# Kernel optimization log

Hardware: AMD Instinct MI355X
Metric: run time of the kernel (lower is better)

## Reference

```python
import jax, jax.numpy as jnp
import numpy as np

N_CLASS, EMB, HID = 32000, 256, 512
B, T = 256, 256


def setup_inputs() -> dict:
    key = jax.random.key(0)
    ks = iter(jax.random.split(key, 64))

    def g(shape, scale=0.02):
        return jax.random.normal(next(ks), shape, jnp.float32) * scale

    inp = {
        "X": jax.random.randint(next(ks), (B, T), 0, N_CLASS),
        "H": g((B, HID)),
        "C": g((B, HID)),
        "E": g((N_CLASS, EMB)),
    }
    # two stacked LSTM cells, gates i/f/o/c; weights stored [in, out] so y = x @ W
    for name in ["i", "f", "o", "c"]:
        inp["W_x" + name] = g((EMB, HID))
        inp["W_h" + name] = g((HID, HID))
        inp["b_" + name] = jnp.ones((HID,), jnp.float32)
        inp["W_x" + name + "1"] = g((EMB, HID))
        inp["W_h" + name + "1"] = g((HID, HID))
        inp["b_" + name + "1"] = jnp.ones((HID,), jnp.float32)
    inp["W_xh"] = g((HID, HID))
    inp["W_hh"] = g((HID, HID))
    inp["b_h"] = jnp.ones((HID,), jnp.float32)
    inp["W_hq"] = g((HID, N_CLASS))
    inp["b_q"] = jnp.ones((N_CLASS,), jnp.float32)
    return inp


def reference(X, H, C, E,
              W_xi, W_hi, b_i, W_xf, W_hf, b_f, W_xo, W_ho, b_o, W_xc, W_hc, b_c,
              W_xi1, W_hi1, b_i1, W_xf1, W_hf1, b_f1, W_xo1, W_ho1, b_o1, W_xc1, W_hc1, b_c1,
              W_xh, W_hh, b_h, W_hq, b_q):
    xs = jnp.swapaxes(E[X], 0, 1)  # [T, B, EMB] time-major, like X.transpose(0,1)

    def step(carry, x_t):
        H, C, H1, C1 = carry
        # first LSTM cell
        I = jax.nn.sigmoid(x_t @ W_xi + H @ W_hi + b_i)
        F = jax.nn.sigmoid(x_t @ W_xf + H @ W_hf + b_f)
        O = jax.nn.sigmoid(x_t @ W_xo + H @ W_ho + b_o)
        Ct = jnp.tanh(x_t @ W_xc + H @ W_hc + b_c)
        C = F * C + I * Ct
        H = O * jnp.tanh(C)
        # inter-layer gated mix (note: H1 is overwritten before the 2nd cell, as in the original)
        H1 = jax.nn.sigmoid(H @ W_xh + H1 @ W_hh + b_h)
        # second LSTM cell
        I1 = jax.nn.sigmoid(x_t @ W_xi1 + H1 @ W_hi1 + b_i1)
        F1 = jax.nn.sigmoid(x_t @ W_xf1 + H1 @ W_hf1 + b_f1)
        O1 = jax.nn.sigmoid(x_t @ W_xo1 + H1 @ W_ho1 + b_o1)
        Ct1 = jnp.tanh(x_t @ W_xc1 + H1 @ W_hc1 + b_c1)
        C1 = F1 * C1 + I1 * Ct1
        H1 = O1 * jnp.tanh(C1)
        return (H, C, H1, C1), None

    # H1 and C1 are initialized from H and C (H1 = H; C1 = C in the original)
    (H, C, H1, C1), _ = jax.lax.scan(step, (H, C, H, C), xs)
    return H1 @ W_hq + b_q  # [B, N_CLASS]
```

## Files before the change

### kernel.cpp

```cpp
#include <hip/hip_runtime.h>
#include <cstdint>
#include <cstddef>

typedef unsigned short u16;
typedef unsigned long long u64;
typedef __attribute__((ext_vector_type(8))) short s16x8;
typedef __attribute__((ext_vector_type(4))) float f32x4;
typedef __attribute__((ext_vector_type(4))) unsigned short u16x4;

#define AGENT __HIP_MEMORY_SCOPE_AGENT

namespace {
constexpr int NWG  = 256;
constexpr int NTHR = 256;
constexpr int Bb   = 256;
constexpr int Tt   = 256;
constexpr int EMB_ = 256;
constexpr int HID_ = 512;
constexpr int NCLS = 32000;

constexpr int OFF_W1  = 0;
constexpr int OFF_W3  = 49152;
constexpr int OFF_W2  = 98304;
constexpr int OFF_DS  = 131072;
constexpr int OFF_DS1 = 139520;
constexpr int OFF_DSM = 147968;
constexpr int OFF_C   = 150144;
constexpr int OFF_C1  = 152192;
constexpr int OFF_B1  = 154240;
constexpr int OFF_B3  = 154368;
constexpr int OFF_B2  = 154496;
constexpr int SMEM_BYTES = 154560;

constexpr size_t WS_FL   = 0;
constexpr size_t WS_DONE = 32768;
constexpr size_t WS_HB0  = 33792;
constexpr size_t WS_HB1  = WS_HB0 + (size_t)Bb * HID_ * 2;
constexpr size_t WS_H1   = WS_HB1 + (size_t)Bb * HID_ * 2;
constexpr size_t WS_HM   = WS_H1 + (size_t)Bb * HID_ * 2;
constexpr size_t WS_XE   = WS_HM + (size_t)Bb * HID_ * 2;
}

struct Params {
  const int* X; const float* Hin; const float* Cin; const float* E;
  const float* Wx[4];  const float* Wh[4];  const float* bg[4];
  const float* Wx1[4]; const float* Wh1[4]; const float* bg1[4];
  const float* Wxh; const float* Whh; const float* bh;
  const float* Whq; const float* bq;
  float* out; char* ws;
};

__device__ __forceinline__ u16 f2bf(float f) {
  union { float f; unsigned u; } v; v.f = f;
  unsigned r = v.u + 0x7FFFu + ((v.u >> 16) & 1u);
  return (u16)(r >> 16);
}
__device__ __forceinline__ float sigm(float x) { return 1.f / (1.f + __expf(-x)); }
__device__ __forceinline__ float tanh_(float x) {
  x = fminf(fmaxf(x, -10.f), 10.f);
  float e = __expf(-2.f * x);
  return (1.f - e) / (1.f + e);
}
__device__ __forceinline__ f32x4 mfma16(s16x8 a, s16x8 b, f32x4 c) {
  return __builtin_amdgcn_mfma_f32_16x16x32_bf16(a, b, c, 0, 0, 0);
}

__device__ __forceinline__ void st8_llc(u16* p2, u64 v) {
  __hip_atomic_store((u64*)p2, v, __ATOMIC_RELAXED, AGENT);
}

#define LD16A(d, b, off)                                                      \
  asm volatile("global_load_dwordx4 %0, %1, off offset:" #off " sc0 sc1"      \
               : "=&v"(d) : "v"(b) : "memory")

__device__ __forceinline__ void ld_h16(s16x8* d, const u16* b) {
  LD16A(d[0],  b, 0);   LD16A(d[1],  b, 64);  LD16A(d[2],  b, 128);
  LD16A(d[3],  b, 192); LD16A(d[4],  b, 256); LD16A(d[5],  b, 320);
  LD16A(d[6],  b, 384); LD16A(d[7],  b, 448); LD16A(d[8],  b, 512);
  LD16A(d[9],  b, 576); LD16A(d[10], b, 640); LD16A(d[11], b, 704);
  LD16A(d[12], b, 768); LD16A(d[13], b, 832); LD16A(d[14], b, 896);
  LD16A(d[15], b, 960);
}
__device__ __forceinline__ void ld_h8a(s16x8* d, const u16* b) {
  LD16A(d[0], b, 0);   LD16A(d[1], b, 64);  LD16A(d[2], b, 128);
  LD16A(d[3], b, 192); LD16A(d[4], b, 256); LD16A(d[5], b, 320);
  LD16A(d[6], b, 384); LD16A(d[7], b, 448);
}
__device__ __forceinline__ void ld_h8b(s16x8* d, const u16* b) {
  LD16A(d[8],  b, 512); LD16A(d[9],  b, 576); LD16A(d[10], b, 640);
  LD16A(d[11], b, 704); LD16A(d[12], b, 768); LD16A(d[13], b, 832);
  LD16A(d[14], b, 896); LD16A(d[15], b, 960);
}
__device__ __forceinline__ void waitld() {
  asm volatile("s_waitcnt vmcnt(0)" ::: "memory");
  __builtin_amdgcn_sched_barrier(0);
}
#define WAITLDN(n) do {                                                       \
  asm volatile("s_waitcnt vmcnt(" #n ")" ::: "memory");                       \
  __builtin_amdgcn_sched_barrier(0); } while (0)

__device__ __forceinline__ void arrive_cnt(int* fl, int c) {
  __syncthreads();
  if (threadIdx.x == 0)
    (void)__hip_atomic_fetch_add(&fl[(c & 7) * 32 + 16], 1, __ATOMIC_RELAXED, AGENT);
}
__device__ __forceinline__ void wait_cnt(int* fl, int ph) {
  const int tgt = ph * 8;
  if (threadIdx.x < 8) {
    for (;;) {
      int v = __hip_atomic_load(&fl[threadIdx.x * 32 + 16], __ATOMIC_RELAXED, AGENT);
      if (!__any(v < tgt)) break;
      __builtin_amdgcn_s_sleep(1);
    }
  }
  __syncthreads();
  __builtin_amdgcn_fence(__ATOMIC_ACQUIRE, "workgroup");
}

__device__ __forceinline__ void groupbar_heavy(int* fl, int slot, int ph) {
  __syncthreads();
  if (threadIdx.x == 0)
    __hip_atomic_store(&fl[slot * 32], ph, __ATOMIC_RELEASE, AGENT);
  if (threadIdx.x < 64) {
    for (;;) {
      int v = __hip_atomic_load(&fl[threadIdx.x * 32], __ATOMIC_RELAXED, AGENT);
      if (!__any(v < ph)) break;
      __builtin_amdgcn_s_sleep(1);
    }
  }
  __syncthreads();
  __builtin_amdgcn_fence(__ATOMIC_ACQUIRE, "agent");
}

__device__ __forceinline__ void donebar(int* dn, int bi) {
  __syncthreads();
  if (threadIdx.x == 0)
    __hip_atomic_store(&dn[bi], 1, __ATOMIC_RELEASE, AGENT);
  for (;;) {
    int v = __hip_atomic_load(&dn[threadIdx.x], __ATOMIC_RELAXED, AGENT);
    if (!__any(v < 1)) break;
    __builtin_amdgcn_s_sleep(1);
  }
  __syncthreads();
  __builtin_amdgcn_fence(__ATOMIC_ACQUIRE, "agent");
}

__device__ __forceinline__ void cell_phase(char* smem, int offW, int offB, int offC,
                                           const u16* Xt, const u16* Hrec, u16* Hdst,
                                           int g, int c, int w, int lane, int tid) {
  const int r = lane & 15, q = lane >> 4;
  const int row0 = w * 16;
  const u16* xrow = Xt + (size_t)(g * 64 + row0 + r) * EMB_;
  const u16* hrow = Hrec + (size_t)(g * 64 + row0 + r) * HID_;
  const u16* wb = (const u16*)(smem + offW) + lane * 8;
  f32x4 acc0 = {0.f, 0.f, 0.f, 0.f}, acc1 = {0.f, 0.f, 0.f, 0.f};
#pragma unroll
  for (int kb = 0; kb < 8; kb++) {
    s16x8 a  = *(const s16x8*)(xrow + kb * 32 + q * 8);
    s16x8 b0 = *(const s16x8*)(wb + (size_t)(kb * 2 + 0) * 512);
    s16x8 b1 = *(const s16x8*)(wb + (size_t)(kb * 2 + 1) * 512);
    acc0 = mfma16(a, b0, acc0);
    acc1 = mfma16(a, b1, acc1);
  }
  s16x8 ha[16];
  ld_h16(ha, hrow + q * 8);
  waitld();
#pragma unroll
  for (int kb = 0; kb < 16; kb++) {
    s16x8 b0 = *(const s16x8*)(wb + (size_t)((kb + 8) * 2 + 0) * 512);
    s16x8 b1 = *(const s16x8*)(wb + (size_t)((kb + 8) * 2 + 1) * 512);
    acc0 = mfma16(ha[kb], b0, acc0);
    acc1 = mfma16(ha[kb], b1, acc1);
  }
  float* Ds = (float*)(smem + OFF_DS);
#pragma unroll
  for (int i = 0; i < 4; i++) {
    Ds[(row0 + q * 4 + i) * 33 + r]      = acc0[i];
    Ds[(row0 + q * 4 + i) * 33 + 16 + r] = acc1[i];
  }
  __syncthreads();
  const float* bs = (const float*)(smem + offB);
  float* Cs = (float*)(smem + offC);
  if (tid < 128) {
    int row = tid >> 1, j0 = (tid & 1) * 4;
    union { u16 h[4]; u64 qv; } pk;
#pragma unroll
    for (int i = 0; i < 4; i++) {
      int j = j0 + i;
      float vi = Ds[row * 33 + 0 + j]  + bs[0 + j];
      float vf = Ds[row * 33 + 8 + j]  + bs[8 + j];
      float vo = Ds[row * 33 + 16 + j] + bs[16 + j];
      float vc = Ds[row * 33 + 24 + j] + bs[24 + j];
      float I = sigm(vi), F = sigm(vf), O = sigm(vo), Ct = tanh_(vc);
      float Cn = F * Cs[row * 8 + j] + I * Ct;
      Cs[row * 8 + j] = Cn;
      pk.h[i] = f2bf(O * tanh_(Cn));
    }
    st8_llc(Hdst + (size_t)(g * 64 + row) * HID_ + c * 8 + j0, pk.qv);
  }
}

__device__ __forceinline__ void cell1_w23(char* smem, const u16* Xt, const u16* Hrec,
                                          u16* Hdst, int g, int c, int lane, int tid) {
  const int wv = (tid >> 6) - 2;
  const int r = lane & 15, q = lane >> 4;
  const u16* wb1 = (const u16*)(smem + OFF_W1) + lane * 8;
  float* D1 = (float*)(smem + OFF_DS1);
#pragma unroll
  for (int blk = 0; blk < 2; blk++) {
    const int rb = wv * 32 + blk * 16;
    const u16* xrow = Xt + (size_t)(g * 64 + rb + r) * EMB_;
    const u16* hrow = Hrec + (size_t)(g * 64 + rb + r) * HID_;
    s16x8 xa[8];
#pragma unroll
    for (int kb = 0; kb < 8; kb++) xa[kb] = *(const s16x8*)(xrow + kb * 32 + q * 8);
    s16x8 hh[16];
    ld_h8a(hh, hrow + q * 8);
    f32x4 a0 = {0.f, 0.f, 0.f, 0.f}, a1 = {0.f, 0.f, 0.f, 0.f};
#pragma unroll
    for (int kb = 0; kb < 8; kb++) {
      a0 = mfma16(xa[kb], *(const s16x8*)(wb1 + (size_t)(kb * 2 + 0) * 512), a0);
      a1 = mfma16(xa[kb], *(const s16x8*)(wb1 + (size_t)(kb * 2 + 1) * 512), a1);
    }
    waitld();
#pragma unroll
    for (int kb = 0; kb < 8; kb++) {
      a0 = mfma16(hh[kb], *(const s16x8*)(wb1 + (size_t)((kb + 8) * 2 + 0) * 512), a0);
      a1 = mfma16(hh[kb], *(const s16x8*)(wb1 + (size_t)((kb + 8) * 2 + 1) * 512), a1);
    }
    ld_h8b(hh, hrow + q * 8);
    waitld();
#pragma unroll
    for (int kb = 8; kb < 16; kb++) {
      a0 = mfma16(hh[kb], *(const s16x8*)(wb1 + (size_t)((kb + 8) * 2 + 0) * 512), a0);
      a1 = mfma16(hh[kb], *(const s16x8*)(wb1 + (size_t)((kb + 8) * 2 + 1) * 512), a1);
    }
#pragma unroll
    for (int i = 0; i < 4; i++) {
      D1[(rb + q * 4 + i) * 33 + r]      = a0[i];
      D1[(rb + q * 4 + i) * 33 + 16 + r] = a1[i];
    }
  }
  const float* bs = (const float*)(smem + OFF_B1);
  float* Cs = (float*)(smem + OFF_C);
  int t2 = tid - 128;
  int row = t2 >> 1, j0 = (t2 & 1) * 4;
  union { u16 h[4]; u64 qv; } pk;
#pragma unroll
  for (int i = 0; i < 4; i++) {
    int j = j0 + i;
    float vi = D1[row * 33 + 0 + j]  + bs[0 + j];
    float vf = D1[row * 33 + 8 + j]  + bs[8 + j];
    float vo = D1[row * 33 + 16 + j] + bs[16 + j];
    float vc = D1[row * 33 + 24 + j] + bs[24 + j];
    float I = sigm(vi), F = sigm(vf), O = sigm(vo), Ct = tanh_(vc);
    float Cn = F * Cs[row * 8 + j] + I * Ct;
    Cs[row * 8 + j] = Cn;
    pk.h[i] = f2bf(O * tanh_(Cn));
  }
  st8_llc(Hdst + (size_t)(g * 64 + row) * HID_ + c * 8 + j0, pk.qv);
}

__device__ __forceinline__ f32x4 mix_part1(char* smem, const u16* Hnew, int g, int c,
                                           int w, int lane) {
  const int r = lane & 15, q = lane >> 4;
  int rbase = g * 64 + (c & 1) * 32 + w * 16 + r;
  const u16* h0 = Hnew + (size_t)rbase * HID_;
  const u16* wb = (const u16*)(smem + OFF_W2) + lane * 8;
  s16x8 ha[16];
  f32x4 acc = {0.f, 0.f, 0.f, 0.f};
  ld_h8a(ha, h0 + q * 8);
  waitld();
#pragma unroll
  for (int kb = 0; kb < 8; kb++)
    acc = mfma16(ha[kb], *(const s16x8*)(wb + (size_t)kb * 512), acc);
  ld_h8b(ha, h0 + q * 8);
  waitld();
#pragma unroll
  for (int kb = 8; kb < 16; kb++)
    acc = mfma16(ha[kb], *(const s16x8*)(wb + (size_t)kb * 512), acc);
  return acc;
}

__device__ __forceinline__ void mix_part2(char* smem, f32x4 acc, const u16* H1old,
                                          u16* H1m, int g, int c, int w, int lane) {
  const int r = lane & 15, q = lane >> 4;
  int rbase = g * 64 + (c & 1) * 32 + w * 16 + r;
  const u16* h1 = H1old + (size_t)rbase * HID_;
  const u16* wb = (const u16*)(smem + OFF_W2) + lane * 8;
  s16x8 hb[16];
  ld_h16(hb, h1 + q * 8);
  __builtin_amdgcn_sched_barrier(0);
  WAITLDN(12);
#pragma unroll
  for (int kb = 0; kb < 4; kb++)
    acc = mfma16(hb[kb], *(const s16x8*)(wb + (size_t)(16 + kb) * 512), acc);
  WAITLDN(8);
#pragma unroll
  for (int kb = 4; kb < 8; kb++)
    acc = mfma16(hb[kb], *(const s16x8*)(wb + (size_t)(16 + kb) * 512), acc);
  WAITLDN(4);
#pragma unroll
  for (int kb = 8; kb < 12; kb++)
    acc = mfma16(hb[kb], *(const s16x8*)(wb + (size_t)(16 + kb) * 512), acc);
  WAITLDN(0);
#pragma unroll
  for (int kb = 12; kb < 16; kb++)
    acc = mfma16(hb[kb], *(const s16x8*)(wb + (size_t)(16 + kb) * 512), acc);
  float* Dm = (float*)(smem + OFF_DSM) + (size_t)w * 16 * 17;
#pragma unroll
  for (int i = 0; i < 4; i++) Dm[(q * 4 + i) * 17 + r] = acc[i];
  const float* b2 = (const float*)(smem + OFF_B2);
  int row2 = lane >> 2, j0 = (lane & 3) * 4;
  union { u16 h[4]; u64 qv; } pk;
#pragma unroll
  for (int i = 0; i < 4; i++)
    pk.h[i] = f2bf(sigm(Dm[row2 * 17 + j0 + i] + b2[j0 + i]));
  st8_llc(H1m + (size_t)(g * 64 + (c & 1) * 32 + w * 16 + row2) * HID_ + (c >> 1) * 16 + j0,
          pk.qv);
}

__global__ __launch_bounds__(NTHR, 1) void lstm_pers(Params p) {
  extern __shared__ char smem[];
  const int tid = threadIdx.x;
  const int bi = blockIdx.x;
  const int w = tid >> 6, lane = tid & 63;
  const int g = bi >> 6, c = bi & 63;
  const int r = lane & 15, q = lane >> 4;

  int* fl = (int*)(p.ws + WS_FL) + g * 64 * 32;
  int* dn = (int*)(p.ws + WS_DONE);
  u16* Hb0 = (u16*)(p.ws + WS_HB0);
  u16* Hb1 = (u16*)(p.ws + WS_HB1);
  u16* H1b = (u16*)(p.ws + WS_H1);
  u16* H1m = (u16*)(p.ws + WS_HM);
  u16* Xe  = (u16*)(p.ws + WS_XE);

  if (tid == 0 && c < 8)
    __hip_atomic_store(&fl[c * 32 + 16], 0, __ATOMIC_RELAXED, AGENT);

  {
    u16* w1 = (u16*)(smem + OFF_W1);
    u16* w3 = (u16*)(smem + OFF_W3);
    int gate = tid >> 6, kk8 = (tid >> 3) & 7, j = tid & 7;
    int cc = gate * 8 + j;
    int n = cc >> 4, rr = cc & 15;
    int hid = c * 8 + j;
    for (int kk = kk8; kk < 768; kk += 8) {
      int kb = kk >> 5, q2 = (kk >> 3) & 3, e = kk & 7;
      size_t dst = ((size_t)(kb * 2 + n) * 64 + q2 * 16 + rr) * 8 + e;
      float s1 = (kk < 256) ? p.Wx[gate][(size_t)kk * HID_ + hid]
                            : p.Wh[gate][(size_t)(kk - 256) * HID_ + hid];
      float s3 = (kk < 256) ? p.Wx1[gate][(size_t)kk * HID_ + hid]
                            : p.Wh1[gate][(size_t)(kk - 256) * HID_ + hid];
      w1[dst] = f2bf(s1);
      w3[dst] = f2bf(s3);
    }
    {
      u16* w2 = (u16*)(smem + OFF_W2);
      int kk16 = tid >> 4, j2 = tid & 15;
      int hid2 = (c >> 1) * 16 + j2;
      for (int kk = kk16; kk < 1024; kk += 16) {
        int kb = kk >> 5, q2 = (kk >> 3) & 3, e = kk & 7;
        size_t dst = ((size_t)kb * 64 + q2 * 16 + j2) * 8 + e;
        float s = (kk < 512) ? p.Wxh[(size_t)kk * HID_ + hid2]
                             : p.Whh[(size_t)(kk - 512) * HID_ + hid2];
        w2[dst] = f2bf(s);
      }
      if (tid < 16) ((float*)(smem + OFF_B2))[tid] = p.bh[(c >> 1) * 16 + tid];
    }
    if (tid < 32) {
      int gt = tid >> 3, jj = tid & 7;
      ((float*)(smem + OFF_B1))[tid] = p.bg[gt][c * 8 + jj];
      ((float*)(smem + OFF_B3))[tid] = p.bg1[gt][c * 8 + jj];
    }
    float* Cs = (float*)(smem + OFF_C);
    float* C1s = (float*)(smem + OFF_C1);
    for (int it = 0; it < 2; it++) {
      int idx = tid + it * 256;
      int row = idx >> 3, j8 = idx & 7;
      float v = p.Cin[(size_t)(g * 64 + row) * HID_ + c * 8 + j8];
      Cs[row * 8 + j8] = v;
      C1s[row * 8 + j8] = v;
    }
  }
  for (int it = 0; it < 2; it++) {
    int idx = bi * 512 + tid + it * 256;
    u16 hv = f2bf(p.Hin[idx]);
    Hb1[idx] = hv;
    H1b[idx] = hv;
  }
  for (int tt = 0; tt < 4; tt++) {
    int t0 = c * 4 + tt;
    for (int pp = 0; pp < 16; pp++) {
      int b = g * 64 + w * 16 + pp;
      int tok = p.X[(size_t)b * Tt + t0];
      const float4* er = (const float4*)(p.E + (size_t)tok * EMB_);
      float4 v = er[lane];
      u16x4 u; u.x = f2bf(v.x); u.y = f2bf(v.y); u.z = f2bf(v.z); u.w = f2bf(v.w);
      *(u16x4*)(Xe + ((size_t)t0 * Bb + b) * EMB_ + lane * 4) = u;
    }
  }
  groupbar_heavy(fl, c, 1);

  int cph = 0;

  cell_phase(smem, OFF_W1, OFF_B1, OFF_C, Xe, Hb1, Hb0, g, c, w, lane, tid);
  arrive_cnt(fl, c); ++cph;

  wait_cnt(fl, cph);
  if (w < 2) {
    f32x4 macc = mix_part1(smem, Hb0, g, c, w, lane);
    mix_part2(smem, macc, H1b, H1m, g, c, w, lane);
  } else {
    cell1_w23(smem, Xe + (size_t)1 * Bb * EMB_, Hb0, Hb1, g, c, lane, tid);
  }
  arrive_cnt(fl, c); ++cph;

  for (int t = 0; t < Tt - 1; t++) {
    const u16* Xt = Xe + (size_t)t * Bb * EMB_;
    {
      const u16* wb3 = (const u16*)(smem + OFF_W3) + lane * 8;
      const u16* xrow = Xt + (size_t)(g * 64 + w * 16 + r) * EMB_;
      f32x4 acc0 = {0.f, 0.f, 0.f, 0.f}, acc1 = {0.f, 0.f, 0.f, 0.f};
      s16x8 xa[8];
#pragma unroll
      for (int kb = 0; kb < 8; kb++) xa[kb] = *(const s16x8*)(xrow + kb * 32 + q * 8);
#pragma unroll
      for (int kb = 0; kb < 8; kb++) {
        acc0 = mfma16(xa[kb], *(const s16x8*)(wb3 + (size_t)(kb * 2 + 0) * 512), acc0);
        acc1 = mfma16(xa[kb], *(const s16x8*)(wb3 + (size_t)(kb * 2 + 1) * 512), acc1);
      }
      wait_cnt(fl, cph);
      const u16* hrow = H1m + (size_t)(g * 64 + w * 16 + r) * HID_;
      s16x8 ha[16];
      ld_h16(ha, hrow + q * 8);
      __builtin_amdgcn_sched_barrier(0);
      WAITLDN(12);
#pragma unroll
      for (int kb = 0; kb < 4; kb++) {
        acc0 = mfma16(ha[kb], *(const s16x8*)(wb3 + (size_t)((kb + 8) * 2 + 0) * 512), acc0);
        acc1 = mfma16(ha[kb], *(const s16x8*)(wb3 + (size_t)((kb + 8) * 2 + 1) * 512), acc1);
      }
      WAITLDN(8);
#pragma unroll
      for (int kb = 4; kb < 8; kb++) {
        acc0 = mfma16(ha[kb], *(const s16x8*)(wb3 + (size_t)((kb + 8) * 2 + 0) * 512), acc0);
        acc1 = mfma16(ha[kb], *(const s16x8*)(wb3 + (size_t)((kb + 8) * 2 + 1) * 512), acc1);
      }
      WAITLDN(4);
#pragma unroll
      for (int kb = 8; kb < 12; kb++) {
        acc0 = mfma16(ha[kb], *(const s16x8*)(wb3 + (size_t)((kb + 8) * 2 + 0) * 512), acc0);
        acc1 = mfma16(ha[kb], *(const s16x8*)(wb3 + (size_t)((kb + 8) * 2 + 1) * 512), acc1);
      }
      WAITLDN(0);
#pragma unroll
      for (int kb = 12; kb < 16; kb++) {
        acc0 = mfma16(ha[kb], *(const s16x8*)(wb3 + (size_t)((kb + 8) * 2 + 0) * 512), acc0);
        acc1 = mfma16(ha[kb], *(const s16x8*)(wb3 + (size_t)((kb + 8) * 2 + 1) * 512), acc1);
      }
      float* Ds = (float*)(smem + OFF_DS);
#pragma unroll
      for (int i = 0; i < 4; i++) {
        Ds[(w * 16 + q * 4 + i) * 33 + r]      = acc0[i];
        Ds[(w * 16 + q * 4 + i) * 33 + 16 + r] = acc1[i];
      }
      __syncthreads();
      if (tid < 128) {
        const float* bs = (const float*)(smem + OFF_B3);
        float* Cs = (float*)(smem + OFF_C1);
        int row = tid >> 1, j0 = (tid & 1) * 4;
        union { u16 h[4]; u64 qv; } pk;
#pragma unroll
        for (int i = 0; i < 4; i++) {
          int j = j0 + i;
          float vi = Ds[row * 33 + 0 + j]  + bs[0 + j];
          float vf = Ds[row * 33 + 8 + j]  + bs[8 + j];
          float vo = Ds[row * 33 + 16 + j] + bs[16 + j];
          float vc = Ds[row * 33 + 24 + j] + bs[24 + j];
          float I = sigm(vi), F = sigm(vf), O = sigm(vo), Ct = tanh_(vc);
          float Cn = F * Cs[row * 8 + j] + I * Ct;
          Cs[row * 8 + j] = Cn;
          pk.h[i] = f2bf(O * tanh_(Cn));
        }
        st8_llc(H1b + (size_t)(g * 64 + row) * HID_ + c * 8 + j0, pk.qv);
      }
      arrive_cnt(fl, c); ++cph;
    }
    {
      const u16* Hnew = (t & 1) ? Hb0 : Hb1;
      u16* Hdst1      = (t & 1) ? Hb1 : Hb0;
      f32x4 macc = {0.f, 0.f, 0.f, 0.f};
      if (w < 2) {
        macc = mix_part1(smem, Hnew, g, c, w, lane);
      } else if (t + 2 < Tt) {
        cell1_w23(smem, Xe + (size_t)(t + 2) * Bb * EMB_, Hnew, Hdst1, g, c, lane, tid);
      }
      wait_cnt(fl, cph);
      if (w < 2) mix_part2(smem, macc, H1b, H1m, g, c, w, lane);
      arrive_cnt(fl, c); ++cph;
    }
  }

  {
    const u16* Xt = Xe + (size_t)(Tt - 1) * Bb * EMB_;
    const u16* wb3 = (const u16*)(smem + OFF_W3) + lane * 8;
    const u16* xrow = Xt + (size_t)(g * 64 + w * 16 + r) * EMB_;
    f32x4 acc0 = {0.f, 0.f, 0.f, 0.f}, acc1 = {0.f, 0.f, 0.f, 0.f};
    s16x8 xa[8];
#pragma unroll
    for (int kb = 0; kb < 8; kb++) xa[kb] = *(const s16x8*)(xrow + kb * 32 + q * 8);
#pragma unroll
    for (int kb = 0; kb < 8; kb++) {
      acc0 = mfma16(xa[kb], *(const s16x8*)(wb3 + (size_t)(kb * 2 + 0) * 512), acc0);
      acc1 = mfma16(xa[kb], *(const s16x8*)(wb3 + (size_t)(kb * 2 + 1) * 512), acc1);
    }
    wait_cnt(fl, cph);
    const u16* hrow = H1m + (size_t)(g * 64 + w * 16 + r) * HID_;
    s16x8 ha[16];
    ld_h16(ha, hrow + q * 8);
    waitld();
#pragma unroll
    for (int kb = 0; kb < 16; kb++) {
      acc0 = mfma16(ha[kb], *(const s16x8*)(wb3 + (size_t)((kb + 8) * 2 + 0) * 512), acc0);
      acc1 = mfma16(ha[kb], *(const s16x8*)(wb3 + (size_t)((kb + 8) * 2 + 1) * 512), acc1);
    }
    float* Ds = (float*)(smem + OFF_DS);
#pragma unroll
    for (int i = 0; i < 4; i++) {
      Ds[(w * 16 + q * 4 + i) * 33 + r]      = acc0[i];
      Ds[(w * 16 + q * 4 + i) * 33 + 16 + r] = acc1[i];
    }
    __syncthreads();
    if (tid < 128) {
      const float* bs = (const float*)(smem + OFF_B3);
      float* Cs = (float*)(smem + OFF_C1);
      int row = tid >> 1, j0 = (tid & 1) * 4;
      union { u16 h[4]; u64 qv; } pk;
#pragma unroll
      for (int i = 0; i < 4; i++) {
        int j = j0 + i;
        float vi = Ds[row * 33 + 0 + j]  + bs[0 + j];
        float vf = Ds[row * 33 + 8 + j]  + bs[8 + j];
        float vo = Ds[row * 33 + 16 + j] + bs[16 + j];
        float vc = Ds[row * 33 + 24 + j] + bs[24 + j];
        float I = sigm(vi), F = sigm(vf), O = sigm(vo), Ct = tanh_(vc);
        float Cn = F * Cs[row * 8 + j] + I * Ct;
        Cs[row * 8 + j] = Cn;
        pk.h[i] = f2bf(O * tanh_(Cn));
      }
      st8_llc(H1b + (size_t)(g * 64 + row) * HID_ + c * 8 + j0, pk.qv);
    }
  }

  donebar(dn, bi);
  if (bi < 250) {
    const int n0 = bi * 128;
    u16* Wf = (u16*)smem;
    for (int idx = tid; idx < 512 * 128; idx += NTHR) {
      int k = idx >> 7, nn2 = idx & 127;
      int nt = nn2 >> 4, rr = nn2 & 15;
      int kb = k >> 5, q2 = (k >> 3) & 3, e = k & 7;
      Wf[((size_t)(kb * 8 + nt) * 64 + q2 * 16 + rr) * 8 + e] =
          f2bf(p.Whq[(size_t)k * NCLS + n0 + nn2]);
    }
    float* bqs = (float*)(smem + OFF_C);
    if (tid < 128) bqs[tid] = p.bq[n0 + tid];
    __syncthreads();
    const int r2 = lane & 15, q2 = lane >> 4;
    for (int mt = 0; mt < 4; mt++) {
      int rowb = mt * 64 + w * 16;
      const u16* arow = H1b + (size_t)(rowb + r2) * HID_;
      f32x4 acc[8];
#pragma unroll
      for (int nt = 0; nt < 8; nt++) acc[nt] = (f32x4){0.f, 0.f, 0.f, 0.f};
      for (int kb = 0; kb < 16; kb++) {
        s16x8 a = *(const s16x8*)(arow + kb * 32 + q2 * 8);
#pragma unroll
        for (int nt = 0; nt < 8; nt++) {
          s16x8 b = *(const s16x8*)((const u16*)Wf + ((size_t)(kb * 8 + nt) * 64 + lane) * 8);
          acc[nt] = mfma16(a, b, acc[nt]);
        }
      }
#pragma unroll
      for (int nt = 0; nt < 8; nt++)
#pragma unroll
        for (int i = 0; i < 4; i++)
          p.out[(size_t)(rowb + q2 * 4 + i) * NCLS + n0 + nt * 16 + r2] =
              acc[nt][i] + bqs[nt * 16 + r2];
    }
  }
}

extern "C" void kernel_launch(void* const* d_in, const int* in_sizes, int n_in,
                              void* d_out, int out_size, void* d_ws, size_t ws_size,
                              hipStream_t stream) {
  (void)in_sizes; (void)n_in; (void)out_size; (void)ws_size;
  Params p;
  p.X   = (const int*)d_in[0];
  p.Hin = (const float*)d_in[1];
  p.Cin = (const float*)d_in[2];
  p.E   = (const float*)d_in[3];
  for (int gidx = 0; gidx < 4; gidx++) {
    int base = 4 + gidx * 6;
    p.Wx[gidx]  = (const float*)d_in[base + 0];
    p.Wh[gidx]  = (const float*)d_in[base + 1];
    p.bg[gidx]  = (const float*)d_in[base + 2];
    p.Wx1[gidx] = (const float*)d_in[base + 3];
    p.Wh1[gidx] = (const float*)d_in[base + 4];
    p.bg1[gidx] = (const float*)d_in[base + 5];
  }
  p.Wxh = (const float*)d_in[28];
  p.Whh = (const float*)d_in[29];
  p.bh  = (const float*)d_in[30];
  p.Whq = (const float*)d_in[31];
  p.bq  = (const float*)d_in[32];
  p.out = (float*)d_out;
  p.ws  = (char*)d_ws;

  hipFuncSetAttribute(reinterpret_cast<const void*>(lstm_pers),
                      hipFuncAttributeMaxDynamicSharedMemorySize, SMEM_BYTES);
  lstm_pers<<<dim3(NWG), dim3(NTHR), SMEM_BYTES, stream>>>(p);
}
```

Before: 3.399 ms.

## Quantize inter-layer hidden states H1 and mix output to uint8 with fp16 MFMA

The second-layer hidden state and the gated mix output are stored as 8-bit unsigned codes (affine for H1, scaled for the sigmoid mix) instead of bf16. Consumers decode the bytes to fp16 and run fp16 MFMAs against fp16 weights, then apply the scale. The zero-point offset is folded into the biases via precomputed column sums of the weights. This halves the bytes exchanged between workgroups on every recurrent step, which targets the latency-bound cross-workgroup traffic, at the cost of extra decode instructions and considerably lower numerical precision.

```diff
diff --git a/kernel.cpp b/kernel.cpp
--- a/kernel.cpp
+++ b/kernel.cpp
@@ -3,9 +3,12 @@
 #include <cstddef>
 
 typedef unsigned short u16;
+typedef unsigned char u8;
 typedef unsigned long long u64;
 typedef __attribute__((ext_vector_type(8))) short s16x8;
+typedef __attribute__((ext_vector_type(8))) _Float16 f16x8;
 typedef __attribute__((ext_vector_type(4))) float f32x4;
+typedef __attribute__((ext_vector_type(4))) unsigned int u32x4;
 typedef __attribute__((ext_vector_type(4))) unsigned short u16x4;
 
 #define AGENT __HIP_MEMORY_SCOPE_AGENT
@@ -18,6 +21,9 @@
 constexpr int EMB_ = 256;
 constexpr int HID_ = 512;
 constexpr int NCLS = 32000;
+
+constexpr float S_HM = 1.0f / 255.0f;
+constexpr float S_H1 = 1.0f / 127.5f;
 
 constexpr int OFF_W1  = 0;
 constexpr int OFF_W3  = 49152;
@@ -36,9 +42,9 @@
 constexpr size_t WS_DONE = 32768;
 constexpr size_t WS_HB0  = 33792;
 constexpr size_t WS_HB1  = WS_HB0 + (size_t)Bb * HID_ * 2;
-constexpr size_t WS_H1   = WS_HB1 + (size_t)Bb * HID_ * 2;
-constexpr size_t WS_HM   = WS_H1 + (size_t)Bb * HID_ * 2;
-constexpr size_t WS_XE   = WS_HM + (size_t)Bb * HID_ * 2;
+constexpr size_t WS_H18  = WS_HB1 + (size_t)Bb * HID_ * 2;
+constexpr size_t WS_HM8  = WS_H18 + (size_t)Bb * HID_;
+constexpr size_t WS_XE   = WS_HM8 + (size_t)Bb * HID_;
 }
 
 struct Params {
@@ -55,6 +61,10 @@
   unsigned r = v.u + 0x7FFFu + ((v.u >> 16) & 1u);
   return (u16)(r >> 16);
 }
+__device__ __forceinline__ u16 f2h(float f) {
+  _Float16 h = (_Float16)f;
+  union { _Float16 h; u16 u; } v; v.h = h; return v.u;
+}
 __device__ __forceinline__ float sigm(float x) { return 1.f / (1.f + __expf(-x)); }
 __device__ __forceinline__ float tanh_(float x) {
   x = fminf(fmaxf(x, -10.f), 10.f);
@@ -64,11 +74,42 @@
 __device__ __forceinline__ f32x4 mfma16(s16x8 a, s16x8 b, f32x4 c) {
   return __builtin_amdgcn_mfma_f32_16x16x32_bf16(a, b, c, 0, 0, 0);
 }
+__device__ __forceinline__ f32x4 mfma16h(f16x8 a, f16x8 b, f32x4 c) {
+  return __builtin_amdgcn_mfma_f32_16x16x32_f16(a, b, c, 0, 0, 0);
+}
+
+__device__ __forceinline__ int permk(int k) {
+  return ((k >> 6) << 6) | (((k >> 3) & 3) << 4) | (((k >> 5) & 1) << 3) | (k & 7);
+}
+
+__device__ __forceinline__ f16x8 dec8(unsigned lo, unsigned hi) {
+  union { unsigned w[4]; f16x8 v; } o;
+  float a, b;
+  asm("v_cvt_f32_ubyte0 %0, %1" : "=v"(a) : "v"(lo));
+  asm("v_cvt_f32_ubyte1 %0, %1" : "=v"(b) : "v"(lo));
+  asm("v_cvt_pkrtz_f16_f32 %0, %1, %2" : "=v"(o.w[0]) : "v"(a), "v"(b));
+  asm("v_cvt_f32_ubyte2 %0, %1" : "=v"(a) : "v"(lo));
+  asm("v_cvt_f32_ubyte3 %0, %1" : "=v"(b) : "v"(lo));
+  asm("v_cvt_pkrtz_f16_f32 %0, %1, %2" : "=v"(o.w[1]) : "v"(a), "v"(b));
+  asm("v_cvt_f32_ubyte0 %0, %1" : "=v"(a) : "v"(hi));
+  asm("v_cvt_f32_ubyte1 %0, %1" : "=v"(b) : "v"(hi));
+  asm("v_cvt_pkrtz_f16_f32 %0, %1, %2" : "=v"(o.w[2]) : "v"(a), "v"(b));
+  asm("v_cvt_f32_ubyte2 %0, %1" : "=v"(a) : "v"(hi));
+  asm("v_cvt_f32_ubyte3 %0, %1" : "=v"(b) : "v"(hi));
+  asm("v_cvt_pkrtz_f16_f32 %0, %1, %2" : "=v"(o.w[3]) : "v"(a), "v"(b));
+  return o.v;
+}
+__device__ __forceinline__ unsigned enc4(float a, float b, float c2, float d) {
+  unsigned ua = (unsigned)a, ub = (unsigned)b, uc = (unsigned)c2, ud = (unsigned)d;
+  return ua | (ub << 8) | (uc << 16) | (ud << 24);
+}
 
 __device__ __forceinline__ void st8_llc(u16* p2, u64 v) {
   __hip_atomic_store((u64*)p2, v, __ATOMIC_RELAXED, AGENT);
 }
-
+__device__ __forceinline__ void st4_llc(u8* pb, unsigned v) {
+  __hip_atomic_store((unsigned*)pb, v, __ATOMIC_RELAXED, AGENT);
+}
 #define LD16A(d, b, off)                                                      \
   asm volatile("global_load_dwordx4 %0, %1, off offset:" #off " sc0 sc1"      \
                : "=&v"(d) : "v"(b) : "memory")
@@ -91,6 +132,11 @@
   LD16A(d[11], b, 704); LD16A(d[12], b, 768); LD16A(d[13], b, 832);
   LD16A(d[14], b, 896); LD16A(d[15], b, 960);
 }
+__device__ __forceinline__ void ld_u8x8(u32x4* d, const u8* b) {
+  LD16A(d[0], b, 0);   LD16A(d[1], b, 64);  LD16A(d[2], b, 128);
+  LD16A(d[3], b, 192); LD16A(d[4], b, 256); LD16A(d[5], b, 320);
+  LD16A(d[6], b, 384); LD16A(d[7], b, 448);
+}
 __device__ __forceinline__ void waitld() {
   asm volatile("s_waitcnt vmcnt(0)" ::: "memory");
   __builtin_amdgcn_sched_barrier(0);
@@ -116,7 +162,6 @@
   __syncthreads();
   __builtin_amdgcn_fence(__ATOMIC_ACQUIRE, "workgroup");
 }
-
 __device__ __forceinline__ void groupbar_heavy(int* fl, int slot, int ph) {
   __syncthreads();
   if (threadIdx.x == 0)
@@ -131,7 +176,6 @@
   __syncthreads();
   __builtin_amdgcn_fence(__ATOMIC_ACQUIRE, "agent");
 }
-
 __device__ __forceinline__ void donebar(int* dn, int bi) {
   __syncthreads();
   if (threadIdx.x == 0)
@@ -157,20 +201,16 @@
 #pragma unroll
   for (int kb = 0; kb < 8; kb++) {
     s16x8 a  = *(const s16x8*)(xrow + kb * 32 + q * 8);
-    s16x8 b0 = *(const s16x8*)(wb + (size_t)(kb * 2 + 0) * 512);
-    s16x8 b1 = *(const s16x8*)(wb + (size_t)(kb * 2 + 1) * 512);
-    acc0 = mfma16(a, b0, acc0);
-    acc1 = mfma16(a, b1, acc1);
+    acc0 = mfma16(a, *(const s16x8*)(wb + (size_t)(kb * 2 + 0) * 512), acc0);
+    acc1 = mfma16(a, *(const s16x8*)(wb + (size_t)(kb * 2 + 1) * 512), acc1);
   }
   s16x8 ha[16];
   ld_h16(ha, hrow + q * 8);
   waitld();
 #pragma unroll
   for (int kb = 0; kb < 16; kb++) {
-    s16x8 b0 = *(const s16x8*)(wb + (size_t)((kb + 8) * 2 + 0) * 512);
-    s16x8 b1 = *(const s16x8*)(wb + (size_t)((kb + 8) * 2 + 1) * 512);
-    acc0 = mfma16(ha[kb], b0, acc0);
-    acc1 = mfma16(ha[kb], b1, acc1);
+    acc0 = mfma16(ha[kb], *(const s16x8*)(wb + (size_t)((kb + 8) * 2 + 0) * 512), acc0);
+    acc1 = mfma16(ha[kb], *(const s16x8*)(wb + (size_t)((kb + 8) * 2 + 1) * 512), acc1);
   }
   float* Ds = (float*)(smem + OFF_DS);
 #pragma unroll
@@ -282,42 +322,56 @@
   return acc;
 }
 
-__device__ __forceinline__ void mix_part2(char* smem, f32x4 acc, const u16* H1old,
-                                          u16* H1m, int g, int c, int w, int lane) {
+__device__ __forceinline__ void mix_part2(char* smem, f32x4 macc, const u8* H18,
+                                          u8* HM8, int g, int c, int w, int lane) {
   const int r = lane & 15, q = lane >> 4;
   int rbase = g * 64 + (c & 1) * 32 + w * 16 + r;
-  const u16* h1 = H1old + (size_t)rbase * HID_;
+  const u8* h1 = H18 + (size_t)rbase * 512 + q * 16;
   const u16* wb = (const u16*)(smem + OFF_W2) + lane * 8;
-  s16x8 hb[16];
-  ld_h16(hb, h1 + q * 8);
+  u32x4 rw[8];
+  ld_u8x8(rw, h1);
   __builtin_amdgcn_sched_barrier(0);
-  WAITLDN(12);
-#pragma unroll
-  for (int kb = 0; kb < 4; kb++)
-    acc = mfma16(hb[kb], *(const s16x8*)(wb + (size_t)(16 + kb) * 512), acc);
-  WAITLDN(8);
-#pragma unroll
-  for (int kb = 4; kb < 8; kb++)
-    acc = mfma16(hb[kb], *(const s16x8*)(wb + (size_t)(16 + kb) * 512), acc);
+  f32x4 acch = {0.f, 0.f, 0.f, 0.f};
+  WAITLDN(6);
+#pragma unroll
+  for (int j = 0; j < 2; j++) {
+    acch = mfma16h(dec8(rw[j].x, rw[j].y), *(const f16x8*)(wb + (size_t)(16 + 2 * j) * 512), acch);
+    acch = mfma16h(dec8(rw[j].z, rw[j].w), *(const f16x8*)(wb + (size_t)(17 + 2 * j) * 512), acch);
+  }
   WAITLDN(4);
 #pragma unroll
-  for (int kb = 8; kb < 12; kb++)
-    acc = mfma16(hb[kb], *(const s16x8*)(wb + (size_t)(16 + kb) * 512), acc);
+  for (int j = 2; j < 4; j++) {
+    acch = mfma16h(dec8(rw[j].x, rw[j].y), *(const f16x8*)(wb + (size_t)(16 + 2 * j) * 512), acch);
+    acch = mfma16h(dec8(rw[j].z, rw[j].w), *(const f16x8*)(wb + (size_t)(17 + 2 * j) * 512), acch);
+  }
+  WAITLDN(2);
+#pragma unroll
+  for (int j = 4; j < 6; j++) {
+    acch = mfma16h(dec8(rw[j].x, rw[j].y), *(const f16x8*)(wb + (size_t)(16 + 2 * j) * 512), acch);
+    acch = mfma16h(dec8(rw[j].z, rw[j].w), *(const f16x8*)(wb + (size_t)(17 + 2 * j) * 512), acch);
+  }
   WAITLDN(0);
 #pragma unroll
-  for (int kb = 12; kb < 16; kb++)
-    acc = mfma16(hb[kb], *(const s16x8*)(wb + (size_t)(16 + kb) * 512), acc);
+  for (int j = 6; j < 8; j++) {
+    acch = mfma16h(dec8(rw[j].x, rw[j].y), *(const f16x8*)(wb + (size_t)(16 + 2 * j) * 512), acch);
+    acch = mfma16h(dec8(rw[j].z, rw[j].w), *(const f16x8*)(wb + (size_t)(17 + 2 * j) * 512), acch);
+  }
+  f32x4 acc;
+#pragma unroll
+  for (int i = 0; i < 4; i++) acc[i] = macc[i] + acch[i] * S_H1;
   float* Dm = (float*)(smem + OFF_DSM) + (size_t)w * 16 * 17;
 #pragma unroll
   for (int i = 0; i < 4; i++) Dm[(q * 4 + i) * 17 + r] = acc[i];
   const float* b2 = (const float*)(smem + OFF_B2);
   int row2 = lane >> 2, j0 = (lane & 3) * 4;
-  union { u16 h[4]; u64 qv; } pk;
-#pragma unroll
-  for (int i = 0; i < 4; i++)
-    pk.h[i] = f2bf(sigm(Dm[row2 * 17 + j0 + i] + b2[j0 + i]));
-  st8_llc(H1m + (size_t)(g * 64 + (c & 1) * 32 + w * 16 + row2) * HID_ + (c >> 1) * 16 + j0,
-          pk.qv);
+  float s0 = sigm(Dm[row2 * 17 + j0 + 0] + b2[j0 + 0]);
+  float s1 = sigm(Dm[row2 * 17 + j0 + 1] + b2[j0 + 1]);
+  float s2 = sigm(Dm[row2 * 17 + j0 + 2] + b2[j0 + 2]);
+  float s3 = sigm(Dm[row2 * 17 + j0 + 3] + b2[j0 + 3]);
+  unsigned pv = enc4(s0 * 255.f + 0.5f, s1 * 255.f + 0.5f,
+                     s2 * 255.f + 0.5f, s3 * 255.f + 0.5f);
+  int colg = (c >> 1) * 16 + j0;
+  st4_llc(HM8 + (size_t)(g * 64 + (c & 1) * 32 + w * 16 + row2) * 512 + permk(colg), pv);
 }
 
 __global__ __launch_bounds__(NTHR, 1) void lstm_pers(Params p) {
@@ -332,8 +386,8 @@
   int* dn = (int*)(p.ws + WS_DONE);
   u16* Hb0 = (u16*)(p.ws + WS_HB0);
   u16* Hb1 = (u16*)(p.ws + WS_HB1);
-  u16* H1b = (u16*)(p.ws + WS_H1);
-  u16* H1m = (u16*)(p.ws + WS_HM);
+  u8* H18  = (u8*)(p.ws + WS_H18);
+  u8* HM8  = (u8*)(p.ws + WS_HM8);
   u16* Xe  = (u16*)(p.ws + WS_XE);
 
   if (tid == 0 && c < 8)
@@ -354,7 +408,7 @@
       float s3 = (kk < 256) ? p.Wx1[gate][(size_t)kk * HID_ + hid]
                             : p.Wh1[gate][(size_t)(kk - 256) * HID_ + hid];
       w1[dst] = f2bf(s1);
-      w3[dst] = f2bf(s3);
+      w3[dst] = (kk < 256) ? f2bf(s3) : f2h(s3);
     }
     {
       u16* w2 = (u16*)(smem + OFF_W2);
@@ -365,9 +419,24 @@
         size_t dst = ((size_t)kb * 64 + q2 * 16 + j2) * 8 + e;
         float s = (kk < 512) ? p.Wxh[(size_t)kk * HID_ + hid2]
                              : p.Whh[(size_t)(kk - 512) * HID_ + hid2];
-        w2[dst] = f2bf(s);
-      }
-      if (tid < 16) ((float*)(smem + OFF_B2))[tid] = p.bh[(c >> 1) * 16 + tid];
+        w2[dst] = (kk < 512) ? f2bf(s) : f2h(s);
+      }
+    }
+    {
+      float* scr = (float*)(smem + OFF_DSM);
+      int col = tid & 15, part = tid >> 4;
+      int hid2 = (c >> 1) * 16 + col;
+      float s = 0.f;
+      for (int k = part * 32; k < part * 32 + 32; k++)
+        s += p.Whh[(size_t)k * HID_ + hid2];
+      scr[col * 16 + part] = s;
+      __syncthreads();
+      if (tid < 16) {
+        float t = 0.f;
+        for (int i2 = 0; i2 < 16; i2++) t += scr[tid * 16 + i2];
+        ((float*)(smem + OFF_B2))[tid] = p.bh[(c >> 1) * 16 + tid] - t;
+      }
+      __syncthreads();
     }
     if (tid < 32) {
       int gt = tid >> 3, jj = tid & 7;
@@ -386,9 +455,11 @@
   }
   for (int it = 0; it < 2; it++) {
     int idx = bi * 512 + tid + it * 256;
-    u16 hv = f2bf(p.Hin[idx]);
-    Hb1[idx] = hv;
-    H1b[idx] = hv;
+    float v = p.Hin[idx];
+    Hb1[idx] = f2bf(v);
+    float vc2 = fminf(fmaxf(v, -0.999f), 0.999f);
+    int row = idx >> 9, k = idx & 511;
+    H18[(size_t)row * 512 + permk(k)] = (u8)((vc2 + 1.f) * 127.5f + 0.5f);
   }
   for (int tt = 0; tt < 4; tt++) {
     int t0 = c * 4 + tt;
@@ -411,7 +482,7 @@
   wait_cnt(fl, cph);
   if (w < 2) {
     f32x4 macc = mix_part1(smem, Hb0, g, c, w, lane);
-    mix_part2(smem, macc, H1b, H1m, g, c, w, lane);
+    mix_part2(smem, macc, H18, HM8, g, c, w, lane);
   } else {
     cell1_w23(smem, Xe + (size_t)1 * Bb * EMB_, Hb0, Hb1, g, c, lane, tid);
   }
@@ -432,33 +503,55 @@
         acc1 = mfma16(xa[kb], *(const s16x8*)(wb3 + (size_t)(kb * 2 + 1) * 512), acc1);
       }
       wait_cnt(fl, cph);
-      const u16* hrow = H1m + (size_t)(g * 64 + w * 16 + r) * HID_;
-      s16x8 ha[16];
-      ld_h16(ha, hrow + q * 8);
+      const u8* hrow8 = HM8 + (size_t)(g * 64 + w * 16 + r) * 512 + q * 16;
+      u32x4 rw[8];
+      ld_u8x8(rw, hrow8);
       __builtin_amdgcn_sched_barrier(0);
-      WAITLDN(12);
-#pragma unroll
-      for (int kb = 0; kb < 4; kb++) {
-        acc0 = mfma16(ha[kb], *(const s16x8*)(wb3 + (size_t)((kb + 8) * 2 + 0) * 512), acc0);
-        acc1 = mfma16(ha[kb], *(const s16x8*)(wb3 + (size_t)((kb + 8) * 2 + 1) * 512), acc1);
-      }
-      WAITLDN(8);
-#pragma unroll
-      for (int kb = 4; kb < 8; kb++) {
-        acc0 = mfma16(ha[kb], *(const s16x8*)(wb3 + (size_t)((kb + 8) * 2 + 0) * 512), acc0);
-        acc1 = mfma16(ha[kb], *(const s16x8*)(wb3 + (size_t)((kb + 8) * 2 + 1) * 512), acc1);
+      f32x4 ah0 = {0.f, 0.f, 0.f, 0.f}, ah1 = {0.f, 0.f, 0.f, 0.f};
+      WAITLDN(6);
+#pragma unroll
+      for (int jj = 0; jj < 2; jj++) {
+        f16x8 f0 = dec8(rw[jj].x, rw[jj].y);
+        f16x8 f1 = dec8(rw[jj].z, rw[jj].w);
+        ah0 = mfma16h(f0, *(const f16x8*)(wb3 + (size_t)((2 * jj + 8) * 2 + 0) * 512), ah0);
+        ah1 = mfma16h(f0, *(const f16x8*)(wb3 + (size_t)((2 * jj + 8) * 2 + 1) * 512), ah1);
+        ah0 = mfma16h(f1, *(const f16x8*)(wb3 + (size_t)((2 * jj + 9) * 2 + 0) * 512), ah0);
+        ah1 = mfma16h(f1, *(const f16x8*)(wb3 + (size_t)((2 * jj + 9) * 2 + 1) * 512), ah1);
       }
       WAITLDN(4);
 #pragma unroll
-      for (int kb = 8; kb < 12; kb++) {
-        acc0 = mfma16(ha[kb], *(const s16x8*)(wb3 + (size_t)((kb + 8) * 2 + 0) * 512), acc0);
-        acc1 = mfma16(ha[kb], *(const s16x8*)(wb3 + (size_t)((kb + 8) * 2 + 1) * 512), acc1);
+      for (int jj = 2; jj < 4; jj++) {
+        f16x8 f0 = dec8(rw[jj].x, rw[jj].y);
+        f16x8 f1 = dec8(rw[jj].z, rw[jj].w);
+        ah0 = mfma16h(f0, *(const f16x8*)(wb3 + (size_t)((2 * jj + 8) * 2 + 0) * 512), ah0);
+        ah1 = mfma16h(f0, *(const f16x8*)(wb3 + (size_t)((2 * jj + 8) * 2 + 1) * 512), ah1);
+        ah0 = mfma16h(f1, *(const f16x8*)(wb3 + (size_t)((2 * jj + 9) * 2 + 0) * 512), ah0);
+        ah1 = mfma16h(f1, *(const f16x8*)(wb3 + (size_t)((2 * jj + 9) * 2 + 1) * 512), ah1);
+      }
+      WAITLDN(2);
+#pragma unroll
+      for (int jj = 4; jj < 6; jj++) {
+        f16x8 f0 = dec8(rw[jj].x, rw[jj].y);
+        f16x8 f1 = dec8(rw[jj].z, rw[jj].w);
+        ah0 = mfma16h(f0, *(const f16x8*)(wb3 + (size_t)((2 * jj + 8) * 2 + 0) * 512), ah0);
+        ah1 = mfma16h(f0, *(const f16x8*)(wb3 + (size_t)((2 * jj + 8) * 2 + 1) * 512), ah1);
+        ah0 = mfma16h(f1, *(const f16x8*)(wb3 + (size_t)((2 * jj + 9) * 2 + 0) * 512), ah0);
+        ah1 = mfma16h(f1, *(const f16x8*)(wb3 + (size_t)((2 * jj + 9) * 2 + 1) * 512), ah1);
       }
       WAITLDN(0);
 #pragma unroll
-      for (int kb = 12; kb < 16; kb++) {
-        acc0 = mfma16(ha[kb], *(const s16x8*)(wb3 + (size_t)((kb + 8) * 2 + 0) * 512), acc0);
-        acc1 = mfma16(ha[kb], *(const s16x8*)(wb3 + (size_t)((kb + 8) * 2 + 1) * 512), acc1);
+      for (int jj = 6; jj < 8; jj++) {
+        f16x8 f0 = dec8(rw[jj].x, rw[jj].y);
+        f16x8 f1 = dec8(rw[jj].z, rw[jj].w);
+        ah0 = mfma16h(f0, *(const f16x8*)(wb3 + (size_t)((2 * jj + 8) * 2 + 0) * 512), ah0);
+        ah1 = mfma16h(f0, *(const f16x8*)(wb3 + (size_t)((2 * jj + 8) * 2 + 1) * 512), ah1);
+        ah0 = mfma16h(f1, *(const f16x8*)(wb3 + (size_t)((2 * jj + 9) * 2 + 0) * 512), ah0);
+        ah1 = mfma16h(f1, *(const f16x8*)(wb3 + (size_t)((2 * jj + 9) * 2 + 1) * 512), ah1);
+      }
+#pragma unroll
+      for (int i = 0; i < 4; i++) {
+        acc0[i] += ah0[i] * S_HM;
+        acc1[i] += ah1[i] * S_HM;
       }
       float* Ds = (float*)(smem + OFF_DS);
 #pragma unroll
@@ -471,7 +564,7 @@
         const float* bs = (const float*)(smem + OFF_B3);
         float* Cs = (float*)(smem + OFF_C1);
         int row = tid >> 1, j0 = (tid & 1) * 4;
-        union { u16 h[4]; u64 qv; } pk;
+        float hv[4];
 #pragma unroll
         for (int i = 0; i < 4; i++) {
           int j = j0 + i;
@@ -482,9 +575,11 @@
           float I = sigm(vi), F = sigm(vf), O = sigm(vo), Ct = tanh_(vc);
           float Cn = F * Cs[row * 8 + j] + I * Ct;
           Cs[row * 8 + j] = Cn;
-          pk.h[i] = f2bf(O * tanh_(Cn));
+          hv[i] = O * tanh_(Cn);
         }
-        st8_llc(H1b + (size_t)(g * 64 + row) * HID_ + c * 8 + j0, pk.qv);
+        unsigned pv = enc4((hv[0] + 1.f) * 127.5f + 0.5f, (hv[1] + 1.f) * 127.5f + 0.5f,
+                           (hv[2] + 1.f) * 127.5f + 0.5f, (hv[3] + 1.f) * 127.5f + 0.5f);
+        st4_llc(H18 + (size_t)(g * 64 + row) * 512 + permk(c * 8 + j0), pv);
       }
       arrive_cnt(fl, c); ++cph;
     }
@@ -498,7 +593,7 @@
         cell1_w23(smem, Xe + (size_t)(t + 2) * Bb * EMB_, Hnew, Hdst1, g, c, lane, tid);
       }
       wait_cnt(fl, cph);
-      if (w < 2) mix_part2(smem, macc, H1b, H1m, g, c, w, lane);
+      if (w < 2) mix_part2(smem, macc, H18, HM8, g, c, w, lane);
       arrive_cnt(fl, c); ++cph;
     }
   }
@@ -517,14 +612,24 @@
       acc1 = mfma16(xa[kb], *(const s16x8*)(wb3 + (size_t)(kb * 2 + 1) * 512), acc1);
     }
     wait_cnt(fl, cph);
-    const u16* hrow = H1m + (size_t)(g * 64 + w * 16 + r) * HID_;
-    s16x8 ha[16];
-    ld_h16(ha, hrow + q * 8);
+    const u8* hrow8 = HM8 + (size_t)(g * 64 + w * 16 + r) * 512 + q * 16;
+    u32x4 rw[8];
+    ld_u8x8(rw, hrow8);
     waitld();
-#pragma unroll
-    for (int kb = 0; kb < 16; kb++) {
-      acc0 = mfma16(ha[kb], *(const s16x8*)(wb3 + (size_t)((kb + 8) * 2 + 0) * 512), acc0);
-      acc1 = mfma16(ha[kb], *(const s16x8*)(wb3 + (size_t)((kb + 8) * 2 + 1) * 512), acc1);
+    f32x4 ah0 = {0.f, 0.f, 0.f, 0.f}, ah1 = {0.f, 0.f, 0.f, 0.f};
+#pragma unroll
+    for (int jj = 0; jj < 8; jj++) {
+      f16x8 f0 = dec8(rw[jj].x, rw[jj].y);
+      f16x8 f1 = dec8(rw[jj].z, rw[jj].w);
+      ah0 = mfma16h(f0, *(const f16x8*)(wb3 + (size_t)((2 * jj + 8) * 2 + 0) * 512), ah0);
+      ah1 = mfma16h(f0, *(const f16x8*)(wb3 + (size_t)((2 * jj + 8) * 2 + 1) * 512), ah1);
+      ah0 = mfma16h(f1, *(const f16x8*)(wb3 + (size_t)((2 * jj + 9) * 2 + 0) * 512), ah0);
+      ah1 = mfma16h(f1, *(const f16x8*)(wb3 + (size_t)((2 * jj + 9) * 2 + 1) * 512), ah1);
+    }
+#pragma unroll
+    for (int i = 0; i < 4; i++) {
+      acc0[i] += ah0[i] * S_HM;
+      acc1[i] += ah1[i] * S_HM;
     }
     float* Ds = (float*)(smem + OFF_DS);
 #pragma unroll
@@ -537,7 +642,7 @@
       const float* bs = (const float*)(smem + OFF_B3);
       float* Cs = (float*)(smem + OFF_C1);
       int row = tid >> 1, j0 = (tid & 1) * 4;
-      union { u16 h[4]; u64 qv; } pk;
+      float hv[4];
 #pragma unroll
       for (int i = 0; i < 4; i++) {
         int j = j0 + i;
@@ -548,39 +653,57 @@
         float I = sigm(vi), F = sigm(vf), O = sigm(vo), Ct = tanh_(vc);
         float Cn = F * Cs[row * 8 + j] + I * Ct;
         Cs[row * 8 + j] = Cn;
-        pk.h[i] = f2bf(O * tanh_(Cn));
-      }
-      st8_llc(H1b + (size_t)(g * 64 + row) * HID_ + c * 8 + j0, pk.qv);
+        hv[i] = O * tanh_(Cn);
+      }
+      unsigned pv = enc4((hv[0] + 1.f) * 127.5f + 0.5f, (hv[1] + 1.f) * 127.5f + 0.5f,
+                         (hv[2] + 1.f) * 127.5f + 0.5f, (hv[3] + 1.f) * 127.5f + 0.5f);
+      st4_llc(H18 + (size_t)(g * 64 + row) * 512 + permk(c * 8 + j0), pv);
     }
   }
 
   donebar(dn, bi);
   if (bi < 250) {
     const int n0 = bi * 128;
-    u16* Wf = (u16*)smem;
+    _Float16* Wf = (_Float16*)smem;
     for (int idx = tid; idx < 512 * 128; idx += NTHR) {
       int k = idx >> 7, nn2 = idx & 127;
       int nt = nn2 >> 4, rr = nn2 & 15;
       int kb = k >> 5, q2 = (k >> 3) & 3, e = k & 7;
       Wf[((size_t)(kb * 8 + nt) * 64 + q2 * 16 + rr) * 8 + e] =
-          f2bf(p.Whq[(size_t)k * NCLS + n0 + nn2]);
+          (_Float16)p.Whq[(size_t)k * NCLS + n0 + nn2];
     }
     float* bqs = (float*)(smem + OFF_C);
-    if (tid < 128) bqs[tid] = p.bq[n0 + tid];
+    __syncthreads();
+    if (tid < 128) {
+      int nt = tid >> 4, rr = tid & 15;
+      float s = 0.f;
+      for (int kb = 0; kb < 16; kb++)
+        for (int q2 = 0; q2 < 4; q2++)
+#pragma unroll
+          for (int e = 0; e < 8; e++)
+            s += (float)Wf[((size_t)(kb * 8 + nt) * 64 + q2 * 16 + rr) * 8 + e];
+      bqs[tid] = p.bq[n0 + tid] - s;
+    }
     __syncthreads();
     const int r2 = lane & 15, q2 = lane >> 4;
     for (int mt = 0; mt < 4; mt++) {
       int rowb = mt * 64 + w * 16;
-      const u16* arow = H1b + (size_t)(rowb + r2) * HID_;
+      const u8* h1base = H18 + (size_t)(rowb + r2) * 512 + q2 * 16;
+      f16x8 haf[16];
+#pragma unroll
+      for (int jj = 0; jj < 8; jj++) {
+        u32x4 rwv = *(const u32x4*)(h1base + jj * 64);
+        haf[2 * jj]     = dec8(rwv.x, rwv.y);
+        haf[2 * jj + 1] = dec8(rwv.z, rwv.w);
+      }
       f32x4 acc[8];
 #pragma unroll
       for (int nt = 0; nt < 8; nt++) acc[nt] = (f32x4){0.f, 0.f, 0.f, 0.f};
       for (int kb = 0; kb < 16; kb++) {
-        s16x8 a = *(const s16x8*)(arow + kb * 32 + q2 * 8);
 #pragma unroll
         for (int nt = 0; nt < 8; nt++) {
-          s16x8 b = *(const s16x8*)((const u16*)Wf + ((size_t)(kb * 8 + nt) * 64 + lane) * 8);
-          acc[nt] = mfma16(a, b, acc[nt]);
+          f16x8 b = *(const f16x8*)(Wf + ((size_t)(kb * 8 + nt) * 64 + lane) * 8);
+          acc[nt] = mfma16h(haf[kb], b, acc[nt]);
         }
       }
 #pragma unroll
@@ -588,7 +711,7 @@
 #pragma unroll
         for (int i = 0; i < 4; i++)
           p.out[(size_t)(rowb + q2 * 4 + i) * NCLS + n0 + nt * 16 + r2] =
-              acc[nt][i] + bqs[nt * 16 + r2];
+              acc[nt][i] * S_H1 + bqs[nt * 16 + r2];
     }
   }
 }
```

Result: faster. 3.167 ms (-6.8%).
